# Kernel tuning notes

Measured on AMD Instinct MI355X. Metric: run time of the kernel, lower is better.

Reference implementation:

```python
import jax, jax.numpy as jnp
import numpy as np

ROUTING_ITERATIONS = 3


def squash(x):
    # squared norm over the capsule output dim
    sq = jnp.sum(x * x, axis=-1, keepdims=True)
    scale = sq / (1.0 + sq)
    return scale * x / jnp.sqrt(sq)


def setup_inputs() -> dict:
    key = jax.random.key(0)
    k1, k2 = jax.random.split(key)
    B, N, IN_C, K, OUT_C = 256, 1152, 8, 10, 16
    u = jax.random.normal(k1, (B, N, IN_C), dtype=jnp.float32)
    W = jax.random.normal(k2, (K, N, IN_C, OUT_C), dtype=jnp.float32)
    return {"u": u, "W": W}


def reference(u, W):
    # u: [B, N, in_c]; W: [K, N, in_c, out_c]
    # torch: u_hat = matmul(u[None,:,:,None,:], W[:,None]) -> [K, B, N, 1, out_c]
    u_hat = jnp.einsum('bni,knio->kbno', u, W)  # [K, B, N, out_c]
    b_ij = jnp.zeros_like(u_hat)
    v_j = None
    for it in range(ROUTING_ITERATIONS):
        c_ij = jax.nn.softmax(b_ij, axis=2)               # softmax over N, per out_c channel
        s_j = jnp.sum(c_ij * u_hat, axis=2, keepdims=True)  # [K, B, 1, out_c]
        v_j = squash(s_j)
        if it < ROUTING_ITERATIONS - 1:
            a_ij = jnp.sum(u_hat * v_j, axis=-1, keepdims=True)  # [K, B, N, 1]
            b_ij = b_ij + a_ij
    # match torch output shape [K, B, 1, 1, out_c]
    return v_j[:, :, :, None, :]
```

## Files before the change

### kernel.cpp

```cpp
#include <hip/hip_runtime.h>
#include <hip/hip_fp16.h>

#define Bsz 256
#define Nn  1152
#define Kk  10
#define NT  384
#define NW  6
#define S4  1156

#define W_ELEMS (Kk*Nn*128)
#define U_ELEMS (Bsz*Nn*8)

typedef _Float16 hf2_t __attribute__((ext_vector_type(2)));

static __device__ __forceinline__ unsigned pkh2(float x, float y) {
    __half2 h = __floats2half2_rn(x, y);
    return *reinterpret_cast<unsigned*>(&h);
}
static __device__ __forceinline__ float fdot2u(unsigned a, unsigned b, float c) {
    union { unsigned u; hf2_t h; } A, B;
    A.u = a; B.u = b;
    return __builtin_amdgcn_fdot2(A.h, B.h, c, false);
}
static __device__ __forceinline__ void wave_lds_fence() {
    __builtin_amdgcn_sched_barrier(0);
    asm volatile("s_waitcnt lgkmcnt(0)" ::: "memory");
    __builtin_amdgcn_sched_barrier(0);
}

#define PERM_LO 0x01000504u
#define PERM_HI 0x03020706u
#define ONE2    0x3C003C00u

__global__ void cvt_kernel(const float* __restrict__ W, const float* __restrict__ u,
                           __half2* __restrict__ Wh, __half2* __restrict__ uh) {
    const int idx = blockIdx.x * blockDim.x + threadIdx.x;
    const int wg = W_ELEMS / 8;
    const float4* p;
    __half2* o;
    if (idx < wg) {
        p = (const float4*)W + (size_t)idx * 2;
        o = Wh + (size_t)idx * 4;
    } else {
        const int j = idx - wg;
        p = (const float4*)u + (size_t)j * 2;
        o = uh + (size_t)j * 4;
    }
    const float4 a = p[0], b = p[1];
    o[0] = __floats2half2_rn(a.x, a.y);
    o[1] = __floats2half2_rn(a.z, a.w);
    o[2] = __floats2half2_rn(b.x, b.y);
    o[3] = __floats2half2_rn(b.z, b.w);
}

template<bool HALF>
__global__ __launch_bounds__(NT, 3)
void digitcaps_kernel(const float* __restrict__ u32, const float* __restrict__ W32,
                      const __half* __restrict__ uh, const __half* __restrict__ Wh,
                      float* __restrict__ out)
{
    const int t    = threadIdx.x;
    const int lane = t & 63;
    const int wav  = t >> 6;
    const int oh   = lane & 1;
    const int pr   = lane >> 1;
    const int bg   = blockIdx.x;
    const int k    = blockIdx.y;
    const int b0   = 2 * bg;
    const int b1   = 2 * bg + 1;

    __shared__ unsigned uhS[8 * S4];
    __shared__ unsigned cS2u[Nn / 2];
    __shared__ float    redS[2][2][NW][20];

    unsigned uh_r[6][4];

    #pragma unroll
    for (int rr = 0; rr < 6; ++rr) {
        const int n = 192 * rr + 32 * wav + pr;
        float a0[8], a1[8];
        #pragma unroll
        for (int o = 0; o < 8; ++o) { a0[o] = 0.f; a1[o] = 0.f; }
        if (HALF) {
            const uint4 uq0 = *(const uint4*)(uh + ((size_t)b0 * Nn + n) * 8);
            const uint4 uq1 = *(const uint4*)(uh + ((size_t)b1 * Nn + n) * 8);
            const unsigned uw0[4] = {uq0.x, uq0.y, uq0.z, uq0.w};
            const unsigned uw1[4] = {uq1.x, uq1.y, uq1.z, uq1.w};
            const __half* wbase = Wh + ((size_t)(k * Nn + n)) * 128 + oh * 8;
            #pragma unroll
            for (int p = 0; p < 4; ++p) {
                const uint4 qa = *(const uint4*)(wbase + (2 * p    ) * 16);
                const uint4 qb = *(const uint4*)(wbase + (2 * p + 1) * 16);
                const unsigned aw[4] = {qa.x, qa.y, qa.z, qa.w};
                const unsigned bw[4] = {qb.x, qb.y, qb.z, qb.w};
                #pragma unroll
                for (int jj = 0; jj < 4; ++jj) {
                    const unsigned wl  = __builtin_amdgcn_perm(aw[jj], bw[jj], PERM_LO);
                    const unsigned wh2 = __builtin_amdgcn_perm(aw[jj], bw[jj], PERM_HI);
                    a0[2*jj]   = fdot2u(wl,  uw0[p], a0[2*jj]);
                    a0[2*jj+1] = fdot2u(wh2, uw0[p], a0[2*jj+1]);
                    a1[2*jj]   = fdot2u(wl,  uw1[p], a1[2*jj]);
                    a1[2*jj+1] = fdot2u(wh2, uw1[p], a1[2*jj+1]);
                }
            }
        } else {
            float ua0[8], ua1[8];
            const float4* up0 = (const float4*)(u32 + ((size_t)b0 * Nn + n) * 8);
            const float4* up1 = (const float4*)(u32 + ((size_t)b1 * Nn + n) * 8);
            const float4 x0 = up0[0], x1 = up0[1];
            const float4 y0 = up1[0], y1 = up1[1];
            ua0[0]=x0.x; ua0[1]=x0.y; ua0[2]=x0.z; ua0[3]=x0.w;
            ua0[4]=x1.x; ua0[5]=x1.y; ua0[6]=x1.z; ua0[7]=x1.w;
            ua1[0]=y0.x; ua1[1]=y0.y; ua1[2]=y0.z; ua1[3]=y0.w;
            ua1[4]=y1.x; ua1[5]=y1.y; ua1[6]=y1.z; ua1[7]=y1.w;
            #pragma unroll
            for (int i = 0; i < 8; ++i) {
                const float4* wp = (const float4*)(W32 + ((size_t)k * Nn + n) * 128) + oh * 2 + i * 4;
                const float4 w0 = wp[0], w1 = wp[1];
                float wv[8];
                wv[0]=w0.x; wv[1]=w0.y; wv[2]=w0.z; wv[3]=w0.w;
                wv[4]=w1.x; wv[5]=w1.y; wv[6]=w1.z; wv[7]=w1.w;
                const float x = ua0[i], y = ua1[i];
                #pragma unroll
                for (int o = 0; o < 8; ++o) { a0[o] += x * wv[o]; a1[o] += y * wv[o]; }
            }
        }
        #pragma unroll
        for (int jj = 0; jj < 4; ++jj) {
            uhS[(oh * 4 + jj) * S4 + n] = pkh2(a0[2*jj], a0[2*jj+1]);
            uh_r[rr][jj] = pkh2(a1[2*jj], a1[2*jj+1]);
        }
    }
    wave_lds_fence();

    float lg0[3] = {0.f, 0.f, 0.f};
    float lg1[6] = {0.f, 0.f, 0.f, 0.f, 0.f, 0.f};
    unsigned vh0[8];
    unsigned vo1[4];
    const int j_s = lane & 7;
    const int g_s = lane >> 3;
    const int l5  = lane >> 5;
    const int l31 = lane & 31;

    #pragma unroll
    for (int it = 0; it < 3; ++it) {
        float m0 = 0.f, m1 = 0.f;
        float c1[6];
        if (it > 0) {
            #pragma unroll
            for (int j = 0; j < 3; ++j) {
                const int n = 384 * j + 192 * l5 + 32 * wav + l31;
                float acc = 0.f;
                #pragma unroll
                for (int jj = 0; jj < 8; ++jj)
                    acc = fdot2u(uhS[jj * S4 + n], vh0[jj], acc);
                lg0[j] += acc;
            }
            #pragma unroll
            for (int rr = 0; rr < 6; ++rr) {
                float acc = 0.f;
                #pragma unroll
                for (int jj = 0; jj < 4; ++jj)
                    acc = fdot2u(uh_r[rr][jj], vo1[jj], acc);
                lg1[rr] += acc + __shfl_xor(acc, 1);
            }
            m0 = fmaxf(fmaxf(lg0[0], lg0[1]), lg0[2]);
            m1 = fmaxf(fmaxf(fmaxf(lg1[0], lg1[1]), fmaxf(lg1[2], lg1[3])),
                       fmaxf(lg1[4], lg1[5]));
            #pragma unroll
            for (int off = 1; off <= 32; off <<= 1) {
                m0 = fmaxf(m0, __shfl_xor(m0, off));
                m1 = fmaxf(m1, __shfl_xor(m1, off));
            }
            #pragma unroll
            for (int j = 0; j < 3; ++j) {
                const int n = 384 * j + 192 * l5 + 32 * wav + l31;
                ((__half*)cS2u)[n] = __float2half(__expf(lg0[j] - m0));
            }
            #pragma unroll
            for (int rr = 0; rr < 6; ++rr) c1[rr] = __expf(lg1[rr] - m1);
            wave_lds_fence();
        } else {
            #pragma unroll
            for (int rr = 0; rr < 6; ++rr) c1[rr] = 1.f;
        }

        float2 sp0 = {0.f, 0.f};
        float dp0 = 0.f;
        #pragma unroll
        for (int cc = 0; cc < 12; ++cc) {
            const int P  = g_s + 8 * cc;
            const int n0 = 192 * (P >> 4) + 32 * wav + 2 * (P & 15);
            const unsigned cp = (it == 0) ? ONE2 : cS2u[n0 >> 1];
            const uint2 q = *(const uint2*)&uhS[j_s * S4 + n0];
            const unsigned px = __builtin_amdgcn_perm(q.x, q.y, PERM_LO);
            const unsigned py = __builtin_amdgcn_perm(q.x, q.y, PERM_HI);
            sp0.x = fdot2u(px, cp, sp0.x);
            sp0.y = fdot2u(py, cp, sp0.y);
            dp0   = fdot2u(cp, ONE2, dp0);
        }
        #pragma unroll
        for (int off = 8; off <= 32; off <<= 1) {
            sp0.x += __shfl_xor(sp0.x, off);
            sp0.y += __shfl_xor(sp0.y, off);
            dp0   += __shfl_xor(dp0,   off);
        }

        float sp1[8] = {0.f, 0.f, 0.f, 0.f, 0.f, 0.f, 0.f, 0.f};
        float dp1 = 0.f;
        #pragma unroll
        for (int q2 = 0; q2 < 3; ++q2) {
            const unsigned cp1 = pkh2(c1[2*q2], c1[2*q2+1]);
            dp1 = fdot2u(cp1, ONE2, dp1);
            #pragma unroll
            for (int jj = 0; jj < 4; ++jj) {
                const unsigned px = __builtin_amdgcn_perm(uh_r[2*q2][jj], uh_r[2*q2+1][jj], PERM_LO);
                const unsigned py = __builtin_amdgcn_perm(uh_r[2*q2][jj], uh_r[2*q2+1][jj], PERM_HI);
                sp1[2*jj]   = fdot2u(px, cp1, sp1[2*jj]);
                sp1[2*jj+1] = fdot2u(py, cp1, sp1[2*jj+1]);
            }
        }
        #pragma unroll
        for (int off = 2; off <= 32; off <<= 1) {
            #pragma unroll
            for (int e = 0; e < 8; ++e) sp1[e] += __shfl_xor(sp1[e], off);
            dp1 += __shfl_xor(dp1, off);
        }

        const int buf = it & 1;
        if (lane < 8) {
            redS[buf][0][wav][2 * j_s    ] = sp0.x;
            redS[buf][0][wav][2 * j_s + 1] = sp0.y;
        }
        if (lane < 2) {
            float2* dst = (float2*)&redS[buf][1][wav][8 * lane];
            dst[0] = make_float2(sp1[0], sp1[1]);
            dst[1] = make_float2(sp1[2], sp1[3]);
            dst[2] = make_float2(sp1[4], sp1[5]);
            dst[3] = make_float2(sp1[6], sp1[7]);
        }
        if (lane == 0) {
            *(float2*)&redS[buf][0][wav][16] = make_float2(dp0, m0);
            *(float2*)&redS[buf][1][wav][16] = make_float2(dp1, m1);
        }
        __syncthreads();

        if (it < 2 || wav == 0) {
            const int bsel = (lane >> 4) & 1;
            const int o    = lane & 15;
            float M = redS[buf][bsel][0][17];
            #pragma unroll
            for (int w = 1; w < NW; ++w) M = fmaxf(M, redS[buf][bsel][w][17]);
            float s = 0.f, d = 0.f;
            #pragma unroll
            for (int w = 0; w < NW; ++w) {
                const float2 dm = *(const float2*)&redS[buf][bsel][w][16];
                const float sc = (it == 0) ? 1.f : __expf(dm.y - M);
                s += sc * redS[buf][bsel][w][o];
                d += sc * dm.x;
            }
            s /= d;
            float s2 = s * s;
            #pragma unroll
            for (int off = 1; off <= 8; off <<= 1) s2 += __shfl_xor(s2, off);
            const float scale = (s2 / (1.f + s2)) * rsqrtf(fmaxf(s2, 1e-30f));
            const float v = s * scale;
            if (it == 2) {
                if (wav == 0 && lane < 32)
                    out[((size_t)k * Bsz + b0 + bsel) * 16 + o] = v;
            } else {
                #pragma unroll
                for (int jj = 0; jj < 8; ++jj)
                    vh0[jj] = pkh2(__shfl(v, 2 * jj), __shfl(v, 2 * jj + 1));
                #pragma unroll
                for (int jj = 0; jj < 4; ++jj)
                    vo1[jj] = pkh2(__shfl(v, 16 + 8 * oh + 2 * jj),
                                   __shfl(v, 16 + 8 * oh + 2 * jj + 1));
            }
        }
    }
}

extern "C" void kernel_launch(void* const* d_in, const int* in_sizes, int n_in,
                              void* d_out, int out_size, void* d_ws, size_t ws_size,
                              hipStream_t stream) {
    const float* u = (const float*)d_in[0];
    const float* W = (const float*)d_in[1];
    float* out = (float*)d_out;
    const size_t need = (size_t)(W_ELEMS + U_ELEMS) * sizeof(__half);
    if (ws_size >= need) {
        __half* Wh = (__half*)d_ws;
        __half* uh = (__half*)((char*)d_ws + (size_t)W_ELEMS * sizeof(__half));
        cvt_kernel<<<dim3((W_ELEMS + U_ELEMS) / 8 / 256), dim3(256), 0, stream>>>(
            W, u, (__half2*)Wh, (__half2*)uh);
        digitcaps_kernel<true><<<dim3(128, 10), dim3(NT), 0, stream>>>(
            nullptr, nullptr, uh, Wh, out);
    } else {
        digitcaps_kernel<false><<<dim3(128, 10), dim3(NT), 0, stream>>>(
            u, W, nullptr, nullptr, out);
    }
}
```

Measured before the change: 128.2 us.

## Double block threads and keep both batch rows' u_hat in LDS

The block size goes from 384 to 768 threads (12 waves), so each wave now owns a contiguous 96-capsule slice instead of interleaved 192-strided rows. Both batch elements' u_hat now live in shared memory instead of one in LDS and one in registers. The routing logits, softmax weights and weighted sums are computed symmetrically for both batch rows, with lane parity choosing the row. The aim is to cut per-thread register pressure and shorten the per-wave serial work, at the cost of about twice the LDS footprint and a larger cross-wave reduction.

```diff
diff --git a/kernel.cpp b/kernel.cpp
--- a/kernel.cpp
+++ b/kernel.cpp
@@ -4,9 +4,9 @@
 #define Bsz 256
 #define Nn  1152
 #define Kk  10
-#define NT  384
-#define NW  6
-#define S4  1156
+#define NT  768
+#define NW  12
+#define S4  1154
 
 #define W_ELEMS (Kk*Nn*128)
 #define U_ELEMS (Bsz*Nn*8)
@@ -54,7 +54,7 @@
 }
 
 template<bool HALF>
-__global__ __launch_bounds__(NT, 3)
+__global__ __launch_bounds__(NT, 6)
 void digitcaps_kernel(const float* __restrict__ u32, const float* __restrict__ W32,
                       const __half* __restrict__ uh, const __half* __restrict__ Wh,
                       float* __restrict__ out)
@@ -69,15 +69,13 @@
     const int b0   = 2 * bg;
     const int b1   = 2 * bg + 1;
 
-    __shared__ unsigned uhS[8 * S4];
-    __shared__ unsigned cS2u[Nn / 2];
-    __shared__ float    redS[2][2][NW][20];
-
-    unsigned uh_r[6][4];
+    __shared__ unsigned uhS2[2][8][S4];
+    __shared__ unsigned cSu[2][Nn / 2];
+    __shared__ float    redS[2][2][NW][18];
 
     #pragma unroll
-    for (int rr = 0; rr < 6; ++rr) {
-        const int n = 192 * rr + 32 * wav + pr;
+    for (int rr = 0; rr < 3; ++rr) {
+        const int n = 96 * wav + 32 * rr + pr;
         float a0[8], a1[8];
         #pragma unroll
         for (int o = 0; o < 8; ++o) { a0[o] = 0.f; a1[o] = 0.f; }
@@ -127,122 +125,84 @@
         }
         #pragma unroll
         for (int jj = 0; jj < 4; ++jj) {
-            uhS[(oh * 4 + jj) * S4 + n] = pkh2(a0[2*jj], a0[2*jj+1]);
-            uh_r[rr][jj] = pkh2(a1[2*jj], a1[2*jj+1]);
+            uhS2[0][oh * 4 + jj][n] = pkh2(a0[2*jj], a0[2*jj+1]);
+            uhS2[1][oh * 4 + jj][n] = pkh2(a1[2*jj], a1[2*jj+1]);
         }
     }
     wave_lds_fence();
 
-    float lg0[3] = {0.f, 0.f, 0.f};
-    float lg1[6] = {0.f, 0.f, 0.f, 0.f, 0.f, 0.f};
-    unsigned vh0[8];
-    unsigned vo1[4];
+    float lg[3] = {0.f, 0.f, 0.f};
+    unsigned vhsel[8];
     const int j_s = lane & 7;
     const int g_s = lane >> 3;
-    const int l5  = lane >> 5;
-    const int l31 = lane & 31;
 
     #pragma unroll
     for (int it = 0; it < 3; ++it) {
-        float m0 = 0.f, m1 = 0.f;
-        float c1[6];
+        float m_w = 0.f;
         if (it > 0) {
             #pragma unroll
-            for (int j = 0; j < 3; ++j) {
-                const int n = 384 * j + 192 * l5 + 32 * wav + l31;
+            for (int rr = 0; rr < 3; ++rr) {
+                const int n = 96 * wav + 32 * rr + pr;
                 float acc = 0.f;
                 #pragma unroll
                 for (int jj = 0; jj < 8; ++jj)
-                    acc = fdot2u(uhS[jj * S4 + n], vh0[jj], acc);
-                lg0[j] += acc;
-            }
-            #pragma unroll
-            for (int rr = 0; rr < 6; ++rr) {
-                float acc = 0.f;
-                #pragma unroll
-                for (int jj = 0; jj < 4; ++jj)
-                    acc = fdot2u(uh_r[rr][jj], vo1[jj], acc);
-                lg1[rr] += acc + __shfl_xor(acc, 1);
-            }
-            m0 = fmaxf(fmaxf(lg0[0], lg0[1]), lg0[2]);
-            m1 = fmaxf(fmaxf(fmaxf(lg1[0], lg1[1]), fmaxf(lg1[2], lg1[3])),
-                       fmaxf(lg1[4], lg1[5]));
-            #pragma unroll
-            for (int off = 1; off <= 32; off <<= 1) {
-                m0 = fmaxf(m0, __shfl_xor(m0, off));
-                m1 = fmaxf(m1, __shfl_xor(m1, off));
-            }
-            #pragma unroll
-            for (int j = 0; j < 3; ++j) {
-                const int n = 384 * j + 192 * l5 + 32 * wav + l31;
-                ((__half*)cS2u)[n] = __float2half(__expf(lg0[j] - m0));
-            }
-            #pragma unroll
-            for (int rr = 0; rr < 6; ++rr) c1[rr] = __expf(lg1[rr] - m1);
+                    acc = fdot2u(uhS2[oh][jj][n], vhsel[jj], acc);
+                lg[rr] += acc;
+            }
+            float m = fmaxf(fmaxf(lg[0], lg[1]), lg[2]);
+            #pragma unroll
+            for (int off = 2; off <= 32; off <<= 1)
+                m = fmaxf(m, __shfl_xor(m, off));
+            m_w = m;
+            #pragma unroll
+            for (int rr = 0; rr < 3; ++rr) {
+                const int n = 96 * wav + 32 * rr + pr;
+                ((__half*)cSu[oh])[n] = __float2half(__expf(lg[rr] - m_w));
+            }
             wave_lds_fence();
-        } else {
-            #pragma unroll
-            for (int rr = 0; rr < 6; ++rr) c1[rr] = 1.f;
-        }
-
-        float2 sp0 = {0.f, 0.f};
-        float dp0 = 0.f;
-        #pragma unroll
-        for (int cc = 0; cc < 12; ++cc) {
-            const int P  = g_s + 8 * cc;
-            const int n0 = 192 * (P >> 4) + 32 * wav + 2 * (P & 15);
-            const unsigned cp = (it == 0) ? ONE2 : cS2u[n0 >> 1];
-            const uint2 q = *(const uint2*)&uhS[j_s * S4 + n0];
-            const unsigned px = __builtin_amdgcn_perm(q.x, q.y, PERM_LO);
-            const unsigned py = __builtin_amdgcn_perm(q.x, q.y, PERM_HI);
-            sp0.x = fdot2u(px, cp, sp0.x);
-            sp0.y = fdot2u(py, cp, sp0.y);
-            dp0   = fdot2u(cp, ONE2, dp0);
+        }
+
+        float2 sp0 = {0.f, 0.f}, sp1 = {0.f, 0.f};
+        float dp0 = 0.f, dp1 = 0.f;
+        #pragma unroll
+        for (int cc = 0; cc < 6; ++cc) {
+            const int n0 = 96 * wav + 2 * (g_s + 8 * cc);
+            unsigned cp0, cp1;
+            if (it == 0) { cp0 = ONE2; cp1 = ONE2; }
+            else { cp0 = cSu[0][n0 >> 1]; cp1 = cSu[1][n0 >> 1]; }
+            const uint2 q0 = *(const uint2*)&uhS2[0][j_s][n0];
+            const uint2 q1 = *(const uint2*)&uhS2[1][j_s][n0];
+            const unsigned px0 = __builtin_amdgcn_perm(q0.x, q0.y, PERM_LO);
+            const unsigned py0 = __builtin_amdgcn_perm(q0.x, q0.y, PERM_HI);
+            const unsigned px1 = __builtin_amdgcn_perm(q1.x, q1.y, PERM_LO);
+            const unsigned py1 = __builtin_amdgcn_perm(q1.x, q1.y, PERM_HI);
+            sp0.x = fdot2u(px0, cp0, sp0.x);
+            sp0.y = fdot2u(py0, cp0, sp0.y);
+            sp1.x = fdot2u(px1, cp1, sp1.x);
+            sp1.y = fdot2u(py1, cp1, sp1.y);
+            dp0   = fdot2u(cp0, ONE2, dp0);
+            dp1   = fdot2u(cp1, ONE2, dp1);
         }
         #pragma unroll
         for (int off = 8; off <= 32; off <<= 1) {
             sp0.x += __shfl_xor(sp0.x, off);
             sp0.y += __shfl_xor(sp0.y, off);
+            sp1.x += __shfl_xor(sp1.x, off);
+            sp1.y += __shfl_xor(sp1.y, off);
             dp0   += __shfl_xor(dp0,   off);
-        }
-
-        float sp1[8] = {0.f, 0.f, 0.f, 0.f, 0.f, 0.f, 0.f, 0.f};
-        float dp1 = 0.f;
-        #pragma unroll
-        for (int q2 = 0; q2 < 3; ++q2) {
-            const unsigned cp1 = pkh2(c1[2*q2], c1[2*q2+1]);
-            dp1 = fdot2u(cp1, ONE2, dp1);
-            #pragma unroll
-            for (int jj = 0; jj < 4; ++jj) {
-                const unsigned px = __builtin_amdgcn_perm(uh_r[2*q2][jj], uh_r[2*q2+1][jj], PERM_LO);
-                const unsigned py = __builtin_amdgcn_perm(uh_r[2*q2][jj], uh_r[2*q2+1][jj], PERM_HI);
-                sp1[2*jj]   = fdot2u(px, cp1, sp1[2*jj]);
-                sp1[2*jj+1] = fdot2u(py, cp1, sp1[2*jj+1]);
-            }
-        }
-        #pragma unroll
-        for (int off = 2; off <= 32; off <<= 1) {
-            #pragma unroll
-            for (int e = 0; e < 8; ++e) sp1[e] += __shfl_xor(sp1[e], off);
-            dp1 += __shfl_xor(dp1, off);
-        }
-
+            dp1   += __shfl_xor(dp1,   off);
+        }
         const int buf = it & 1;
         if (lane < 8) {
             redS[buf][0][wav][2 * j_s    ] = sp0.x;
             redS[buf][0][wav][2 * j_s + 1] = sp0.y;
-        }
-        if (lane < 2) {
-            float2* dst = (float2*)&redS[buf][1][wav][8 * lane];
-            dst[0] = make_float2(sp1[0], sp1[1]);
-            dst[1] = make_float2(sp1[2], sp1[3]);
-            dst[2] = make_float2(sp1[4], sp1[5]);
-            dst[3] = make_float2(sp1[6], sp1[7]);
-        }
-        if (lane == 0) {
-            *(float2*)&redS[buf][0][wav][16] = make_float2(dp0, m0);
-            *(float2*)&redS[buf][1][wav][16] = make_float2(dp1, m1);
-        }
+            redS[buf][1][wav][2 * j_s    ] = sp1.x;
+            redS[buf][1][wav][2 * j_s + 1] = sp1.y;
+        }
+        if (lane == 0)
+            *(float2*)&redS[buf][0][wav][16] = make_float2(dp0, m_w);
+        if (lane == 1)
+            *(float2*)&redS[buf][1][wav][16] = make_float2(dp1, m_w);
         __syncthreads();
 
         if (it < 2 || wav == 0) {
@@ -271,11 +231,8 @@
             } else {
                 #pragma unroll
                 for (int jj = 0; jj < 8; ++jj)
-                    vh0[jj] = pkh2(__shfl(v, 2 * jj), __shfl(v, 2 * jj + 1));
-                #pragma unroll
-                for (int jj = 0; jj < 4; ++jj)
-                    vo1[jj] = pkh2(__shfl(v, 16 + 8 * oh + 2 * jj),
-                                   __shfl(v, 16 + 8 * oh + 2 * jj + 1));
+                    vhsel[jj] = pkh2(__shfl(v, 16 * oh + 2 * jj),
+                                     __shfl(v, 16 * oh + 2 * jj + 1));
             }
         }
     }
```

New measurement: 115.0 us. -10.3%, faster.
